# Optimization experiments

Hardware: AMD Instinct MI355X
Metric: run time of the kernel (lower is better)

## Reference

```python
import jax, jax.numpy as jnp
import numpy as np
from jax import lax

# config constants (from init_kwargs)
B = 256            # batch of voxels
NPC = 40           # compartments (T2 spectrum grid)
N_ECHOES = 32      # echo train length
T1 = 1000.0        # ms
TAU = 10.0         # echo spacing (ms); epg_signal halves it internally
TR = 3000.0        # repetition time (ms)
SIZE = 3 * N_ECHOES + 1  # EPG state dimension (97)


def _build_S(n):
    """Static EPG shift matrix, exactly as torch fill_S."""
    size = 3 * n + 1
    S = np.zeros((size, size), np.float32)
    S[0, 2] = 1.0
    S[1, 0] = 1.0
    S[2, 5] = 1.0
    S[3, 3] = 1.0
    for o in range(2, n + 1):
        off1 = (o - 1 - 1) * 3 + 2
        off2 = (o + 1 - 1) * 3 + 3
        if off1 <= size:
            S[3 * o - 2, off1 - 1] = 1.0
        if off2 <= size:
            S[3 * o - 1, off2 - 1] = 1.0
        S[3 * o, 3 * o] = 1.0
    return S


def _block_idx(n):
    """Row/col indices of T: T[0,0] plus n copies of the 3x3 block T0 on the diagonal."""
    rows = [0]
    cols = [0]
    for k in range(n):
        for a in range(3):
            for b in range(3):
                rows.append(1 + 3 * k + a)
                cols.append(1 + 3 * k + b)
    return np.asarray(rows), np.asarray(cols)


_S_NP = _build_S(N_ECHOES)
_ROWS, _COLS = _block_idx(N_ECHOES)
_IDX = np.arange(SIZE)
_E1_MASK_NP = (_IDX >= 1) & ((_IDX - 1) % 3 == 2)  # positions holding exp(-tau*R1)


def setup_inputs() -> dict:
    key = jax.random.key(0)
    k1, k2, k3 = jax.random.split(key, 3)
    # refocusing angles in degrees (realistic CPMG range)
    refoc_angle = 120.0 + 60.0 * jax.random.uniform(k1, (B,), dtype=jnp.float32)
    # T2 values in ms
    t2s = 10.0 + 1990.0 * jax.random.uniform(k2, (B, NPC), dtype=jnp.float32)
    # positive compartment weights
    weights = 0.05 + jax.random.uniform(k3, (B, NPC), dtype=jnp.float32)
    return {"refoc_angle": refoc_angle, "t2s": t2s, "weights": weights}


def _epg_forward(refoc_angle, t2s, weights):
    n, size = N_ECHOES, SIZE
    S = jnp.asarray(_S_NP)
    e1_mask = jnp.asarray(_E1_MASK_NP)
    rad = jnp.float32(np.pi / 180.0)
    alpha = refoc_angle * rad          # (B,) refocusing flip in radians
    alpha_exc = alpha / 2.0            # excitation flip = flip/2

    # T (rotation) matrix per batch element: block-diagonal with T0(alpha)
    def build_T(a):
        c2 = jnp.cos(a / 2.0) ** 2
        s2 = jnp.sin(a / 2.0) ** 2
        s = jnp.sin(a)
        c = jnp.cos(a)
        T0 = jnp.stack([
            jnp.stack([c2, s2, s]),
            jnp.stack([s2, c2, -s]),
            jnp.stack([-0.5 * s, 0.5 * s, c]),
        ])  # (3,3)
        vals = jnp.concatenate([jnp.ones((1,), T0.dtype), jnp.tile(T0.reshape(-1), n)])
        return jnp.zeros((size, size), T0.dtype).at[_ROWS, _COLS].set(vals)

    T = jax.vmap(build_T)(alpha)  # (B, size, size)

    # R is diagonal: d = [e2, (e2,e2,e1) * n] with e2=exp(-tau*R2), e1=exp(-tau*R1)
    tau = jnp.float32(TAU / 2.0)
    r2 = 1.0 / t2s                                   # (B, NPC) rates
    r1 = jnp.float32(1.0 / T1)
    e2 = jnp.exp(-tau * r2)                          # (B, NPC)
    e1 = jnp.exp(-tau * r1)                          # scalar
    d = jnp.where(e1_mask, e1, e2[..., None])        # (B, NPC, size)

    # E = (R S) T (R S) = diag(d) @ (S T) @ diag(d) @ S
    M = jnp.einsum('ij,bjk->bik', S, T)                       # (B, size, size)
    Md = M[:, None, :, :] * d[:, :, None, :]                   # (B, NPC, size, size)
    E = d[..., None] * jnp.einsum('bcik,kj->bcij', Md, S)      # (B, NPC, size, size)

    # initial state x0 = [sin(alpha_exc), 0, cos(alpha_exc), 0, ...]
    x0 = (jnp.zeros(d.shape, d.dtype)
          .at[..., 0].set(jnp.sin(alpha_exc)[:, None])
          .at[..., 2].set(jnp.cos(alpha_exc)[:, None]))

    def step(x, _):
        x = jnp.einsum('bcij,bcj->bci', E, x)
        return x, x[..., 0]

    _, H = lax.scan(step, x0, None, length=n)  # (n, B, NPC) echo amplitudes

    # faithful to source: factor uses TR / rate (rate = 1/T1)
    factor = 1.0 - jnp.exp(-jnp.float32(TR) / r1)
    sig = factor * jnp.einsum('nbc,bc->bn', H, weights)  # (B, n)
    return sig / sig[:, :1]


def reference(refoc_angle, t2s, weights):
    return _epg_forward(refoc_angle, t2s, weights)
```

## Files before the change

### kernel.cpp

```cpp
#include <hip/hip_runtime.h>
#include <hip/hip_bf16.h>


#define NB 256
#define NPC 40
#define NECH 32
#define SZ 97

__device__ __forceinline__ float bf16_at(const void* p, int i) {
    return __bfloat162float(((const __hip_bfloat16*)p)[i]);
}
__device__ __forceinline__ float f32_at(const void* p, int i) {
    return ((const float*)p)[i];
}

__global__ __launch_bounds__(64, 1) void epg_kernel(
    const void* __restrict__ refoc,
    const void* __restrict__ t2,
    const void* __restrict__ wts,
    float* __restrict__ out)
{
    const int b = blockIdx.x;
    const int tid = threadIdx.x;
    __shared__ float Hs[NECH][NPC];

    bool in_f32 = false;
    #pragma unroll
    for (int i = 0; i < 32; i += 2) {
        const float v = bf16_at(t2, i);
        if (!(v >= 9.0f && v <= 2100.0f)) in_f32 = true;
    }

    const float adeg = in_f32 ? f32_at(refoc, b) : bf16_at(refoc, b);
    float t2v = 1000.0f, wt = 0.0f;
    if (tid < NPC) {
        t2v = in_f32 ? f32_at(t2,  b * NPC + tid) : bf16_at(t2,  b * NPC + tid);
        wt  = in_f32 ? f32_at(wts, b * NPC + tid) : bf16_at(wts, b * NPC + tid);
    }
    t2v = fminf(fmaxf(t2v, 1.0f), 1.0e6f);

    const float alpha = adeg * 0.017453292519943295f;
    const float sh = sinf(0.5f * alpha);
    const float ch = cosf(0.5f * alpha);
    const float sA = sinf(alpha);
    const float cA = cosf(alpha);
    const float c2 = ch * ch;
    const float s2 = sh * sh;
    const float e1  = 0.9950124791926823f;
    const float e12 = 0.9900498337491681f;
    const float e2  = expf(-5.0f / t2v);
    const float e22 = e2 * e2;

    const float M11 = c2 * e22;
    const float M12 = s2 * e22;
    const float M13 = sA * e12;
    const float M31 = 0.5f * sA * e22;
    const float M33 = cA * e12;

    const float we = wt * e2;

    float v[SZ];
    #pragma unroll
    for (int i = 0; i < SZ; ++i) v[i] = 0.0f;
    v[0] = e2 * ch;
    v[1] = c2 * (e2 * sh);
    v[2] = s2 * (e2 * sh);
    v[3] = -0.5f * sA * (e2 * sh);

    #pragma unroll
    for (int e = 0; e < NECH; ++e) {
        if (tid < NPC) Hs[e][tid] = we * v[2];
        if (e == NECH - 1) break;

        #pragma unroll
        for (int p = 94; p >= 7; p -= 3) v[p] = v[p - 6];
        v[4] = v[0];
        v[1] = v[2];
        #pragma unroll
        for (int p = 2; p <= 89; p += 3) v[p] = v[p + 6];
        v[92] = 0.0f;
        v[95] = 0.0f;
        v[0] = e22 * v[2];

        #pragma unroll
        for (int k = 0; k < 32; ++k) {
            const float a  = v[1 + 3 * k];
            const float bb = v[2 + 3 * k];
            const float zz = v[3 + 3 * k];
            v[1 + 3 * k] = M11 * a + M12 * bb + M13 * zz;
            v[2 + 3 * k] = M12 * a + M11 * bb - M13 * zz;
            v[3 + 3 * k] = M31 * (bb - a) + M33 * zz;
        }
    }

    __syncthreads();

    const int e = tid & 31;
    float sum = 0.0f;
    #pragma unroll
    for (int c = 0; c < NPC; ++c) sum += Hs[e][c];
    const float sum0 = __shfl(sum, 0, 64);
    if (tid < NECH) out[b * NECH + tid] = sum / sum0;
}

extern "C" void kernel_launch(void* const* d_in, const int* in_sizes, int n_in,
                              void* d_out, int out_size, void* d_ws, size_t ws_size,
                              hipStream_t stream) {
    const void* refoc = d_in[0];
    const void* t2s   = d_in[1];
    const void* wts   = d_in[2];
    float* out = (float*)d_out;
    epg_kernel<<<NB, 64, 0, stream>>>(refoc, t2s, wts, out);
}
```

Measured before the change: 69.90 us.

## Distribute EPG state across 16 lanes per compartment with shuffle-based shifts

Each compartment's 97-element EPG state vector, previously held in one thread's registers, is now split across 16 lanes with two 3-element blocks per lane. The per-echo shift becomes cross-lane shuffles instead of register moves, and the block is widened to 640 threads. This removes the register pressure and the serial 32-block update per thread, and uses every lane instead of leaving 24 of 64 idle, at the cost of shuffle latency on each echo step. Each lane also assumes that the only nonzero states lie within the tracked range.

```diff
diff --git a/kernel.cpp b/kernel.cpp
--- a/kernel.cpp
+++ b/kernel.cpp
@@ -5,7 +5,8 @@
 #define NB 256
 #define NPC 40
 #define NECH 32
-#define SZ 97
+#define LPC 16
+#define TPB (NPC * LPC)
 
 __device__ __forceinline__ float bf16_at(const void* p, int i) {
     return __bfloat162float(((const __hip_bfloat16*)p)[i]);
@@ -14,14 +15,16 @@
     return ((const float*)p)[i];
 }
 
-__global__ __launch_bounds__(64, 1) void epg_kernel(
+__global__ __launch_bounds__(TPB, 1) void epg_kernel(
     const void* __restrict__ refoc,
     const void* __restrict__ t2,
     const void* __restrict__ wts,
     float* __restrict__ out)
 {
-    const int b = blockIdx.x;
+    const int b   = blockIdx.x;
     const int tid = threadIdx.x;
+    const int c   = tid >> 4;
+    const int j   = tid & 15;
     __shared__ float Hs[NECH][NPC];
 
     bool in_f32 = false;
@@ -32,11 +35,8 @@
     }
 
     const float adeg = in_f32 ? f32_at(refoc, b) : bf16_at(refoc, b);
-    float t2v = 1000.0f, wt = 0.0f;
-    if (tid < NPC) {
-        t2v = in_f32 ? f32_at(t2,  b * NPC + tid) : bf16_at(t2,  b * NPC + tid);
-        wt  = in_f32 ? f32_at(wts, b * NPC + tid) : bf16_at(wts, b * NPC + tid);
-    }
+    float t2v = in_f32 ? f32_at(t2,  b * NPC + c) : bf16_at(t2,  b * NPC + c);
+    const float wt = in_f32 ? f32_at(wts, b * NPC + c) : bf16_at(wts, b * NPC + c);
     t2v = fminf(fmaxf(t2v, 1.0f), 1.0e6f);
 
     const float alpha = adeg * 0.017453292519943295f;
@@ -46,7 +46,6 @@
     const float cA = cosf(alpha);
     const float c2 = ch * ch;
     const float s2 = sh * sh;
-    const float e1  = 0.9950124791926823f;
     const float e12 = 0.9900498337491681f;
     const float e2  = expf(-5.0f / t2v);
     const float e22 = e2 * e2;
@@ -56,51 +55,55 @@
     const float M13 = sA * e12;
     const float M31 = 0.5f * sA * e22;
     const float M33 = cA * e12;
+    const float we  = wt * e2;
 
-    const float we = wt * e2;
+    float Fp0 = 0.0f, Fp1 = 0.0f, Fm0 = 0.0f, Fm1 = 0.0f, Z0 = 0.0f, Z1 = 0.0f;
+    float f0 = 0.0f;
+    if (j == 0) {
+        const float esh = e2 * sh;
+        Fp0 = c2 * esh;
+        Fm0 = s2 * esh;
+        Z0  = -0.5f * sA * esh;
+        f0  = e2 * ch;
+    }
 
-    float v[SZ];
-    #pragma unroll
-    for (int i = 0; i < SZ; ++i) v[i] = 0.0f;
-    v[0] = e2 * ch;
-    v[1] = c2 * (e2 * sh);
-    v[2] = s2 * (e2 * sh);
-    v[3] = -0.5f * sA * (e2 * sh);
+    const int upL = (j >= 1)  ? j - 1 : 0;
+    const int dnL = (j <= 14) ? j + 1 : 15;
 
     #pragma unroll
     for (int e = 0; e < NECH; ++e) {
-        if (tid < NPC) Hs[e][tid] = we * v[2];
+        if (j == 0) Hs[e][c] = we * Fm0;
         if (e == NECH - 1) break;
 
-        #pragma unroll
-        for (int p = 94; p >= 7; p -= 3) v[p] = v[p - 6];
-        v[4] = v[0];
-        v[1] = v[2];
-        #pragma unroll
-        for (int p = 2; p <= 89; p += 3) v[p] = v[p + 6];
-        v[92] = 0.0f;
-        v[95] = 0.0f;
-        v[0] = e22 * v[2];
+        const float uFp0 = __shfl(Fp0, upL, LPC);
+        const float uFp1 = __shfl(Fp1, upL, LPC);
+        const float dFm0 = __shfl(Fm0, dnL, LPC);
+        const float dFm1 = __shfl(Fm1, dnL, LPC);
 
-        #pragma unroll
-        for (int k = 0; k < 32; ++k) {
-            const float a  = v[1 + 3 * k];
-            const float bb = v[2 + 3 * k];
-            const float zz = v[3 + 3 * k];
-            v[1 + 3 * k] = M11 * a + M12 * bb + M13 * zz;
-            v[2 + 3 * k] = M12 * a + M11 * bb - M13 * zz;
-            v[3 + 3 * k] = M31 * (bb - a) + M33 * zz;
-        }
+        const float nFp0 = (j == 0)  ? Fm0 : uFp0;
+        const float nFp1 = (j == 0)  ? f0  : uFp1;
+        const float nFm0 = (j == 15) ? 0.0f : dFm0;
+        const float nFm1 = (j == 15) ? 0.0f : dFm1;
+        f0 = e22 * dFm0;
+
+        Fp0 = M11 * nFp0 + M12 * nFm0 + M13 * Z0;
+        Fm0 = M12 * nFp0 + M11 * nFm0 - M13 * Z0;
+        Z0  = M31 * (nFm0 - nFp0) + M33 * Z0;
+        Fp1 = M11 * nFp1 + M12 * nFm1 + M13 * Z1;
+        Fm1 = M12 * nFp1 + M11 * nFm1 - M13 * Z1;
+        Z1  = M31 * (nFm1 - nFp1) + M33 * Z1;
     }
 
     __syncthreads();
 
-    const int e = tid & 31;
-    float sum = 0.0f;
-    #pragma unroll
-    for (int c = 0; c < NPC; ++c) sum += Hs[e][c];
-    const float sum0 = __shfl(sum, 0, 64);
-    if (tid < NECH) out[b * NECH + tid] = sum / sum0;
+    if (tid < 64) {
+        const int e = tid & 31;
+        float sum = 0.0f;
+        #pragma unroll
+        for (int cc = 0; cc < NPC; ++cc) sum += Hs[e][cc];
+        const float sum0 = __shfl(sum, 0, 64);
+        if (tid < NECH) out[b * NECH + tid] = sum / sum0;
+    }
 }
 
 extern "C" void kernel_launch(void* const* d_in, const int* in_sizes, int n_in,
@@ -110,5 +113,5 @@
     const void* t2s   = d_in[1];
     const void* wts   = d_in[2];
     float* out = (float*)d_out;
-    epg_kernel<<<NB, 64, 0, stream>>>(refoc, t2s, wts, out);
+    epg_kernel<<<NB, TPB, 0, stream>>>(refoc, t2s, wts, out);
 }
```

Result: faster. 60.04 us (-14.1%).
